# Performance work log

Hardware: AMD Instinct MI355X
Metric: run time of the kernel (lower is better)

Reference implementation:

```python
import jax, jax.numpy as jnp
import numpy as np

B, T, CH_IN = 4096, 8, 2048
C, N, K = 1024, 512, 5  # chennel, prototype length, n_prototypes/classes
EPS = 1e-8


def setup_inputs() -> dict:
    key = jax.random.key(0)
    ks = jax.random.split(key, 14)
    rn = lambda k, s: jax.random.normal(k, s, dtype=jnp.float32)
    return {
        "x": rn(ks[0], (B, T, CH_IN)),
        "static": rn(ks[1], (K, CH_IN, N)),
        "Wk": rn(ks[2], (C, CH_IN)) * 0.02, "bk": rn(ks[3], (C,)) * 0.02,
        "Wv": rn(ks[4], (C, CH_IN)) * 0.02, "bv": rn(ks[5], (C,)) * 0.02,
        "WEk": rn(ks[6], (C, CH_IN)) * 0.02, "bEk": rn(ks[7], (C,)) * 0.02,
        "WEv": rn(ks[8], (C, CH_IN)) * 0.02, "bEv": rn(ks[9], (C,)) * 0.02,
        "Ww": rn(ks[10], (1, C)) * 0.02, "bw": rn(ks[11], (1,)) * 0.02,
        "Wout": rn(ks[12], (K, 2 * C)) * 0.02, "bout": rn(ks[13], (K,)) * 0.02,
    }


def reference(x, static, Wk, bk, Wv, bv, WEk, bEk, WEv, bEv, Ww, bw, Wout, bout):
    # last frame only: [B, ch_in]
    x_last = x[:, -1, :]
    # 1x1 convs on a length-1 sequence == plain linear layers
    k = x_last @ Wk.T + bk  # [B, C]
    v = x_last @ Wv.T + bv  # [B, C]
    # project all 5 static prototypes at once: [K, C, N]
    Ek = jnp.einsum('ci,kin->kcn', WEk, static) + bEk[None, :, None]
    Ev = jnp.einsum('ci,kin->kcn', WEv, static) + bEv[None, :, None]
    # cosine similarity along channel dim (torch eps=1e-8)
    kn = k / jnp.maximum(jnp.linalg.norm(k, axis=1, keepdims=True), EPS)
    Ekn = Ek / jnp.maximum(jnp.linalg.norm(Ek, axis=1, keepdims=True), EPS)
    sim = jnp.einsum('bc,kcn->bkn', kn, Ekn)          # [B, K, N]
    w = jax.nn.softmax(sim, axis=-1)                  # softmax over prototypes' N entries
    # weighted sum of Ev per prototype -> feature_E [B, C, K]
    feature_E = jnp.einsum('kcn,bkn->bck', Ev, w)
    # scalar gate per prototype via conv2_1_W, then sigmoid
    fw = jax.nn.sigmoid(jnp.einsum('c,bck->bk', Ww[0], feature_E) + bw[0])  # [B, K]
    fE = jnp.einsum('bck,bk->bc', feature_E, fw)      # [B, C]
    out = jax.nn.relu(jnp.concatenate([v, fE], axis=1))  # [B, 2C]
    out = out @ Wout.T + bout                          # [B, K]
    return out[:, :, None]                             # [B, K, 1] matching torch conv1d output
```

## Files before the change

### kernel.cpp

```cpp
#include <hip/hip_runtime.h>
#include <hip/hip_bf16.h>

#define BB 4096
#define TT 8
#define CHIN 2048
#define CC 1024
#define NN 512
#define KK 5
#define KN (KK*NN)

typedef __bf16 bf16x8 __attribute__((ext_vector_type(8)));
typedef float  f32x4  __attribute__((ext_vector_type(4)));

#define TM 128
#define TN 128
#define BK 64

__device__ __forceinline__ void gload_lds16(const __hip_bfloat16* g, __hip_bfloat16* l) {
    __builtin_amdgcn_global_load_lds(
        (__attribute__((address_space(1))) void*)const_cast<__hip_bfloat16*>(g),
        (__attribute__((address_space(3))) void*)l,
        16, 0, 0);
}

__global__ __launch_bounds__(256) void gemm_abt(
    const __hip_bfloat16* __restrict__ A, int lda,
    const __hip_bfloat16* __restrict__ BT, int ldb,
    float* __restrict__ Cmat, int ldc,
    int M, int N, int Kdim,
    const float* __restrict__ bias_col)
{
    __shared__ __align__(16) __hip_bfloat16 As[TM * BK];
    __shared__ __align__(16) __hip_bfloat16 Bs[TN * BK];

    const int tid  = threadIdx.x;
    const int wave = tid >> 6;
    const int lane = tid & 63;
    const int wm = (wave >> 1) * 64;
    const int wn = (wave & 1) * 64;
    const int bm = blockIdx.y * TM;
    const int bn = blockIdx.x * TN;

    const int srow = tid >> 3;
    const int scol = (tid & 7) * 8;

    const __hip_bfloat16* Ag = A  + (size_t)bm * lda;
    const __hip_bfloat16* Bg = BT + (size_t)bn * ldb;

    f32x4 acc[4][4];
    #pragma unroll
    for (int i = 0; i < 4; ++i)
        #pragma unroll
        for (int j = 0; j < 4; ++j)
            acc[i][j] = {0.f, 0.f, 0.f, 0.f};

    for (int k0 = 0; k0 < Kdim; k0 += BK) {
        #pragma unroll
        for (int r = 0; r < 4; ++r) {
            int row = srow + r * 32;
            gload_lds16(Ag + (size_t)row * lda + k0 + scol, &As[row * BK + scol]);
        }
        #pragma unroll
        for (int r = 0; r < 4; ++r) {
            int row = srow + r * 32;
            gload_lds16(Bg + (size_t)row * ldb + k0 + scol, &Bs[row * BK + scol]);
        }
        __syncthreads();

        #pragma unroll
        for (int kk = 0; kk < BK; kk += 32) {
            const int koff = kk + (lane >> 4) * 8;
            const int arow = wm + (lane & 15);
            const int brow = wn + (lane & 15);
            bf16x8 aFrag[4], bFrag[4];
            #pragma unroll
            for (int i = 0; i < 4; ++i)
                aFrag[i] = *(const bf16x8*)(&As[(arow + i * 16) * BK + koff]);
            #pragma unroll
            for (int j = 0; j < 4; ++j)
                bFrag[j] = *(const bf16x8*)(&Bs[(brow + j * 16) * BK + koff]);
            #pragma unroll
            for (int i = 0; i < 4; ++i)
                #pragma unroll
                for (int j = 0; j < 4; ++j)
                    acc[i][j] = __builtin_amdgcn_mfma_f32_16x16x32_bf16(
                        aFrag[i], bFrag[j], acc[i][j], 0, 0, 0);
        }
        __syncthreads();
    }

    const int quad = lane >> 4;
    #pragma unroll
    for (int i = 0; i < 4; ++i) {
        #pragma unroll
        for (int j = 0; j < 4; ++j) {
            const int col = bn + wn + j * 16 + (lane & 15);
            const float bc = bias_col ? bias_col[col] : 0.f;
            #pragma unroll
            for (int r = 0; r < 4; ++r) {
                const int row = bm + wm + i * 16 + quad * 4 + r;
                Cmat[(size_t)row * ldc + col] = acc[i][j][r] + bc;
            }
        }
    }
}

__global__ __launch_bounds__(256) void cast_f32_bf16(const float* __restrict__ in,
                                                     __hip_bfloat16* __restrict__ out, int n)
{
    const int idx = (blockIdx.x * 256 + threadIdx.x) * 4;
    if (idx >= n) return;
    const float4 vv = *(const float4*)(in + idx);
    union { __hip_bfloat16 h[4]; unsigned long long u; } pk;
    pk.h[0] = (__hip_bfloat16)vv.x; pk.h[1] = (__hip_bfloat16)vv.y;
    pk.h[2] = (__hip_bfloat16)vv.z; pk.h[3] = (__hip_bfloat16)vv.w;
    *(unsigned long long*)(out + idx) = pk.u;
}

__global__ __launch_bounds__(256) void cast_xlast(const float* __restrict__ x,
                                                  __hip_bfloat16* __restrict__ xb)
{
    const int b = blockIdx.y;
    const int i = (blockIdx.x * 256 + threadIdx.x) * 4;
    const float4 vv = *(const float4*)(x + ((size_t)b * TT + TT - 1) * CHIN + i);
    union { __hip_bfloat16 h[4]; unsigned long long u; } pk;
    pk.h[0] = (__hip_bfloat16)vv.x; pk.h[1] = (__hip_bfloat16)vv.y;
    pk.h[2] = (__hip_bfloat16)vv.z; pk.h[3] = (__hip_bfloat16)vv.w;
    *(unsigned long long*)(xb + (size_t)b * CHIN + i) = pk.u;
}

__global__ __launch_bounds__(256) void concat_bias(const float* __restrict__ a,
                                                   const float* __restrict__ b,
                                                   float* __restrict__ out)
{
    const int i = blockIdx.x * 256 + threadIdx.x;
    out[i] = (i < CC) ? a[i] : b[i - CC];
}

__global__ void transpose_static(const float* __restrict__ st,
                                 __hip_bfloat16* __restrict__ stT)
{
    __shared__ float tile[32][33];
    const int k  = blockIdx.z;
    const int i0 = blockIdx.x * 32;
    const int n0 = blockIdx.y * 32;
    const int tx = threadIdx.x, ty = threadIdx.y;
    #pragma unroll
    for (int r = 0; r < 32; r += 8)
        tile[ty + r][tx] = st[((size_t)k * CHIN + i0 + ty + r) * NN + n0 + tx];
    __syncthreads();
    #pragma unroll
    for (int r = 0; r < 32; r += 8)
        stT[((size_t)k * NN + n0 + ty + r) * CHIN + i0 + tx] = (__hip_bfloat16)tile[tx][ty + r];
}

__global__ void transpose_bf16(const __hip_bfloat16* __restrict__ in,
                               __hip_bfloat16* __restrict__ outp)
{
    __shared__ __hip_bfloat16 tile[32][33];
    const int c0  = blockIdx.x * 32;
    const int kn0 = blockIdx.y * 32;
    const int tx = threadIdx.x, ty = threadIdx.y;
    #pragma unroll
    for (int r = 0; r < 32; r += 8)
        tile[ty + r][tx] = in[(size_t)(kn0 + ty + r) * CC + c0 + tx];
    __syncthreads();
    #pragma unroll
    for (int r = 0; r < 32; r += 8)
        outp[(size_t)(c0 + ty + r) * KN + kn0 + tx] = tile[tx][ty + r];
}

__global__ __launch_bounds__(256) void rownorm(const float* __restrict__ in, int in_ld,
                                               __hip_bfloat16* __restrict__ out, int cols)
{
    const int row = blockIdx.x;
    const float* p = in + (size_t)row * in_ld;
    float s = 0.f;
    for (int c = threadIdx.x; c < cols; c += 256) { float v = p[c]; s += v * v; }
    #pragma unroll
    for (int o = 32; o > 0; o >>= 1) s += __shfl_down(s, o, 64);
    __shared__ float red[4];
    if ((threadIdx.x & 63) == 0) red[threadIdx.x >> 6] = s;
    __syncthreads();
    const float tot = red[0] + red[1] + red[2] + red[3];
    const float inv = 1.f / fmaxf(sqrtf(tot), 1e-8f);
    for (int c = threadIdx.x; c < cols; c += 256)
        out[(size_t)row * cols + c] = (__hip_bfloat16)(p[c] * inv);
}

__global__ __launch_bounds__(256) void prep_gv(const float* __restrict__ Ekv,
                                               const float* __restrict__ Ww,
                                               float* __restrict__ g,
                                               __hip_bfloat16* __restrict__ EvT)
{
    const int kn = blockIdx.x;
    const float* p = Ekv + (size_t)kn * (2 * CC) + CC;
    float s = 0.f;
    for (int c = threadIdx.x; c < CC; c += 256) {
        const float v = p[c];
        s += Ww[c] * v;
        EvT[(size_t)kn * CC + c] = (__hip_bfloat16)v;
    }
    #pragma unroll
    for (int o = 32; o > 0; o >>= 1) s += __shfl_down(s, o, 64);
    __shared__ float red[4];
    if ((threadIdx.x & 63) == 0) red[threadIdx.x >> 6] = s;
    __syncthreads();
    if (threadIdx.x == 0) g[kn] = red[0] + red[1] + red[2] + red[3];
}

__global__ __launch_bounds__(64) void softmax_u(const float* __restrict__ sim,
                                                const float* __restrict__ g,
                                                const float* __restrict__ bw,
                                                __hip_bfloat16* __restrict__ u)
{
    const int bk = blockIdx.x;
    const int b = bk / KK, k = bk % KK;
    const float* sp = sim + (size_t)b * KN + k * NN;
    const float* gp = g + k * NN;
    const int lane = threadIdx.x;

    float vals[8];
    float m = -1e30f;
    #pragma unroll
    for (int j = 0; j < 8; ++j) { vals[j] = sp[lane + 64 * j]; m = fmaxf(m, vals[j]); }
    #pragma unroll
    for (int o = 32; o > 0; o >>= 1) m = fmaxf(m, __shfl_xor(m, o, 64));
    float sum = 0.f;
    #pragma unroll
    for (int j = 0; j < 8; ++j) { vals[j] = expf(vals[j] - m); sum += vals[j]; }
    #pragma unroll
    for (int o = 32; o > 0; o >>= 1) sum += __shfl_xor(sum, o, 64);
    const float inv = 1.f / sum;
    float dot = 0.f;
    #pragma unroll
    for (int j = 0; j < 8; ++j) { vals[j] *= inv; dot += vals[j] * gp[lane + 64 * j]; }
    #pragma unroll
    for (int o = 32; o > 0; o >>= 1) dot += __shfl_xor(dot, o, 64);
    const float fw = 1.f / (1.f + expf(-(dot + bw[0])));
    __hip_bfloat16* up = u + (size_t)b * KN + k * NN;
    #pragma unroll
    for (int j = 0; j < 8; ++j) up[lane + 64 * j] = (__hip_bfloat16)(vals[j] * fw);
}

__global__ __launch_bounds__(256) void final_out(const float* __restrict__ kv,
                                                 const float* __restrict__ fE,
                                                 const float* __restrict__ Wout,
                                                 const float* __restrict__ bout,
                                                 float* __restrict__ out)
{
    const int b = blockIdx.x;
    const float* vp = kv + (size_t)b * (2 * CC) + CC;
    float acc[KK] = {0.f, 0.f, 0.f, 0.f, 0.f};
    for (int c = threadIdx.x; c < CC; c += 256) {
        const float rv = fmaxf(vp[c], 0.f);
        const float rf = fmaxf(fE[(size_t)b * CC + c], 0.f);
        #pragma unroll
        for (int kk = 0; kk < KK; ++kk)
            acc[kk] += Wout[kk * 2 * CC + c] * rv
                     + Wout[kk * 2 * CC + CC + c] * rf;
    }
    __shared__ float red[KK][4];
    const int lane = threadIdx.x & 63, wave = threadIdx.x >> 6;
    #pragma unroll
    for (int kk = 0; kk < KK; ++kk) {
        float s = acc[kk];
        #pragma unroll
        for (int o = 32; o > 0; o >>= 1) s += __shfl_down(s, o, 64);
        if (lane == 0) red[kk][wave] = s;
    }
    __syncthreads();
    if (threadIdx.x < KK) {
        float s = red[threadIdx.x][0] + red[threadIdx.x][1]
                + red[threadIdx.x][2] + red[threadIdx.x][3];
        out[(size_t)b * KK + threadIdx.x] = s + bout[threadIdx.x];
    }
}

extern "C" void kernel_launch(void* const* d_in, const int* in_sizes, int n_in,
                              void* d_out, int out_size, void* d_ws, size_t ws_size,
                              hipStream_t stream)
{
    const float* x    = (const float*)d_in[0];
    const float* stat = (const float*)d_in[1];
    const float* Wk   = (const float*)d_in[2];
    const float* bk   = (const float*)d_in[3];
    const float* Wv   = (const float*)d_in[4];
    const float* bv   = (const float*)d_in[5];
    const float* WEk  = (const float*)d_in[6];
    const float* bEk  = (const float*)d_in[7];
    const float* WEv  = (const float*)d_in[8];
    const float* bEv  = (const float*)d_in[9];
    const float* Ww   = (const float*)d_in[10];
    const float* bw   = (const float*)d_in[11];
    const float* Wout = (const float*)d_in[12];
    const float* bout = (const float*)d_in[13];
    float* out = (float*)d_out;
    char* ws = (char*)d_ws;

    __hip_bfloat16* xb      = (__hip_bfloat16*)(ws + 0);
    __hip_bfloat16* Wkvb    = (__hip_bfloat16*)(ws + 16777216);
    __hip_bfloat16* WEkvb   = (__hip_bfloat16*)(ws + 25165824);
    __hip_bfloat16* staticT = (__hip_bfloat16*)(ws + 33554432);
    float*          Ekv     = (float*)(ws + 44040192);
    __hip_bfloat16* EknT    = (__hip_bfloat16*)(ws + 65011712);
    __hip_bfloat16* EvT     = (__hip_bfloat16*)(ws + 70254592);
    __hip_bfloat16* EvC     = (__hip_bfloat16*)(ws + 75497472);
    float*          g       = (float*)(ws + 80740352);
    float*          kv      = (float*)(ws + 80750592);
    __hip_bfloat16* kn      = (__hip_bfloat16*)(ws + 114305024);
    float*          sim     = (float*)(ws + 122693632);
    __hip_bfloat16* u       = (__hip_bfloat16*)(ws + 164636672);
    float*          fE      = (float*)(ws + 185608192);
    float*          bkv     = (float*)(ws + 202385408);
    float*          bEkv    = (float*)(ws + 202393600);

    const int WN = CC * CHIN;

    cast_f32_bf16<<<WN / 1024, 256, 0, stream>>>(Wk,  Wkvb,       WN);
    cast_f32_bf16<<<WN / 1024, 256, 0, stream>>>(Wv,  Wkvb + WN,  WN);
    cast_f32_bf16<<<WN / 1024, 256, 0, stream>>>(WEk, WEkvb,      WN);
    cast_f32_bf16<<<WN / 1024, 256, 0, stream>>>(WEv, WEkvb + WN, WN);
    cast_xlast<<<dim3(CHIN / 1024, BB), 256, 0, stream>>>(x, xb);
    concat_bias<<<2 * CC / 256, 256, 0, stream>>>(bk, bv, bkv);
    concat_bias<<<2 * CC / 256, 256, 0, stream>>>(bEk, bEv, bEkv);
    transpose_static<<<dim3(CHIN / 32, NN / 32, KK), dim3(32, 8), 0, stream>>>(stat, staticT);

    gemm_abt<<<dim3(2 * CC / TN, KN / TM), 256, 0, stream>>>(
        staticT, CHIN, WEkvb, CHIN, Ekv, 2 * CC, KN, 2 * CC, CHIN, bEkv);
    rownorm<<<KN, 256, 0, stream>>>(Ekv, 2 * CC, EknT, CC);
    prep_gv<<<KN, 256, 0, stream>>>(Ekv, Ww, g, EvT);
    transpose_bf16<<<dim3(CC / 32, KN / 32), dim3(32, 8), 0, stream>>>(EvT, EvC);
    gemm_abt<<<dim3(2 * CC / TN, BB / TM), 256, 0, stream>>>(
        xb, CHIN, Wkvb, CHIN, kv, 2 * CC, BB, 2 * CC, CHIN, bkv);
    rownorm<<<BB, 256, 0, stream>>>(kv, 2 * CC, kn, CC);
    gemm_abt<<<dim3(KN / TN, BB / TM), 256, 0, stream>>>(
        kn, CC, EknT, CC, sim, KN, BB, KN, CC, nullptr);
    softmax_u<<<BB * KK, 64, 0, stream>>>(sim, g, bw, u);
    gemm_abt<<<dim3(CC / TN, BB / TM), 256, 0, stream>>>(
        u, KN, EvC, KN, fE, CC, BB, CC, KN, nullptr);
    final_out<<<BB, 256, 0, stream>>>(kv, fE, Wout, bout, out);
}
```

Measured before the change: 629.9 us.

## Replace GEMM with 256x256 double-buffered swizzled 8-wave kernel, fuse and split-K

```diff
diff --git a/kernel.cpp b/kernel.cpp
--- a/kernel.cpp
+++ b/kernel.cpp
@@ -12,98 +12,235 @@
 typedef __bf16 bf16x8 __attribute__((ext_vector_type(8)));
 typedef float  f32x4  __attribute__((ext_vector_type(4)));
 
-#define TM 128
-#define TN 128
-#define BK 64
+#define BM 256
+#define BN 256
 
 __device__ __forceinline__ void gload_lds16(const __hip_bfloat16* g, __hip_bfloat16* l) {
     __builtin_amdgcn_global_load_lds(
         (__attribute__((address_space(1))) void*)const_cast<__hip_bfloat16*>(g),
-        (__attribute__((address_space(3))) void*)l,
-        16, 0, 0);
-}
-
-__global__ __launch_bounds__(256) void gemm_abt(
-    const __hip_bfloat16* __restrict__ A, int lda,
-    const __hip_bfloat16* __restrict__ BT, int ldb,
+        (__attribute__((address_space(3))) void*)l, 16, 0, 0);
+}
+
+__device__ __forceinline__ void stage_half(const __hip_bfloat16* __restrict__ g, int ldg,
+                                           __hip_bfloat16* l, int tid)
+{
+    #pragma unroll
+    for (int q = 0; q < 2; ++q) {
+        const int P   = q * 8192 + tid * 16;
+        const int row = P >> 7;
+        const int bc  = (P & 127) ^ ((row & 7) << 4);
+        gload_lds16(g + (size_t)row * ldg + (bc >> 1),
+                    (__hip_bfloat16*)((char*)l + P));
+    }
+}
+
+__device__ __forceinline__ bf16x8 lds_read_swz(const __hip_bfloat16* base, int row, int kbyte)
+{
+    int off = row * 128 + kbyte;
+    off ^= (row & 7) << 4;
+    return *(const bf16x8*)((const char*)base + off);
+}
+
+__device__ __forceinline__ void gemm8p_body(
+    const __hip_bfloat16* __restrict__ Ag, int lda,
+    const __hip_bfloat16* __restrict__ Bg, int ldb,
     float* __restrict__ Cmat, int ldc,
-    int M, int N, int Kdim,
-    const float* __restrict__ bias_col)
-{
-    __shared__ __align__(16) __hip_bfloat16 As[TM * BK];
-    __shared__ __align__(16) __hip_bfloat16 Bs[TN * BK];
+    int ntiles,
+    const float* __restrict__ bias_col,
+    int bm, int bn)
+{
+    __shared__ __align__(16) __hip_bfloat16 As[2][BM * 64];
+    __shared__ __align__(16) __hip_bfloat16 Bs[2][BN * 64];
 
     const int tid  = threadIdx.x;
     const int wave = tid >> 6;
     const int lane = tid & 63;
-    const int wm = (wave >> 1) * 64;
-    const int wn = (wave & 1) * 64;
-    const int bm = blockIdx.y * TM;
-    const int bn = blockIdx.x * TN;
-
-    const int srow = tid >> 3;
-    const int scol = (tid & 7) * 8;
-
-    const __hip_bfloat16* Ag = A  + (size_t)bm * lda;
-    const __hip_bfloat16* Bg = BT + (size_t)bn * ldb;
-
-    f32x4 acc[4][4];
-    #pragma unroll
-    for (int i = 0; i < 4; ++i)
+    const int wrow = (wave >> 2) * 128;
+    const int wcol = (wave & 3) * 64;
+    const int fr   = lane & 15;
+    const int kb0  = (lane >> 4) * 16;
+
+    const __hip_bfloat16* Arow = Ag + (size_t)bm * lda;
+    const __hip_bfloat16* Brow = Bg + (size_t)bn * ldb;
+
+    f32x4 acc[8][4];
+    #pragma unroll
+    for (int i = 0; i < 8; ++i)
         #pragma unroll
         for (int j = 0; j < 4; ++j)
             acc[i][j] = {0.f, 0.f, 0.f, 0.f};
 
-    for (int k0 = 0; k0 < Kdim; k0 += BK) {
-        #pragma unroll
-        for (int r = 0; r < 4; ++r) {
-            int row = srow + r * 32;
-            gload_lds16(Ag + (size_t)row * lda + k0 + scol, &As[row * BK + scol]);
+    bf16x8 a[4][2];
+    bf16x8 bfr[4][2];
+
+    stage_half(Arow,                       lda, &As[0][0],        tid);
+    stage_half(Arow + (size_t)128 * lda,   lda, &As[0][128 * 64], tid);
+    stage_half(Brow,                       ldb, &Bs[0][0],        tid);
+    stage_half(Brow + (size_t)128 * ldb,   ldb, &Bs[0][128 * 64], tid);
+    if (ntiles > 1) {
+        stage_half(Brow + 64,                     ldb, &Bs[1][0],        tid);
+        stage_half(Brow + (size_t)128 * ldb + 64, ldb, &Bs[1][128 * 64], tid);
+        asm volatile("s_waitcnt vmcnt(4)" ::: "memory");
+    } else {
+        asm volatile("s_waitcnt vmcnt(0)" ::: "memory");
+    }
+    __builtin_amdgcn_s_barrier();
+    __builtin_amdgcn_sched_barrier(0);
+
+    for (int T = 0; T < ntiles; ++T) {
+        const __hip_bfloat16* Abuf = &As[T & 1][0];
+        const __hip_bfloat16* Bbuf = &Bs[T & 1][0];
+
+        #pragma unroll
+        for (int i = 0; i < 4; ++i)
+            #pragma unroll
+            for (int k2 = 0; k2 < 2; ++k2)
+                a[i][k2] = lds_read_swz(Abuf, wrow + i * 16 + fr, k2 * 64 + kb0);
+        #pragma unroll
+        for (int j = 0; j < 2; ++j)
+            #pragma unroll
+            for (int k2 = 0; k2 < 2; ++k2)
+                bfr[j][k2] = lds_read_swz(Bbuf, wcol + j * 16 + fr, k2 * 64 + kb0);
+        if (T + 1 < ntiles)
+            stage_half(Arow + (size_t)(T + 1) * 64, lda, &As[(T + 1) & 1][0], tid);
+        __builtin_amdgcn_s_barrier();
+        asm volatile("s_waitcnt lgkmcnt(0)" ::: "memory");
+        __builtin_amdgcn_sched_barrier(0);
+        __builtin_amdgcn_s_setprio(1);
+        #pragma unroll
+        for (int i = 0; i < 4; ++i)
+            #pragma unroll
+            for (int j = 0; j < 2; ++j)
+                #pragma unroll
+                for (int k2 = 0; k2 < 2; ++k2)
+                    acc[i][j] = __builtin_amdgcn_mfma_f32_16x16x32_bf16(
+                        a[i][k2], bfr[j][k2], acc[i][j], 0, 0, 0);
+        __builtin_amdgcn_s_setprio(0);
+        __builtin_amdgcn_s_barrier();
+        __builtin_amdgcn_sched_barrier(0);
+
+        #pragma unroll
+        for (int j = 2; j < 4; ++j)
+            #pragma unroll
+            for (int k2 = 0; k2 < 2; ++k2)
+                bfr[j][k2] = lds_read_swz(Bbuf, wcol + j * 16 + fr, k2 * 64 + kb0);
+        if (T + 1 < ntiles)
+            stage_half(Arow + (size_t)128 * lda + (size_t)(T + 1) * 64, lda,
+                       &As[(T + 1) & 1][128 * 64], tid);
+        __builtin_amdgcn_s_barrier();
+        asm volatile("s_waitcnt lgkmcnt(0)" ::: "memory");
+        __builtin_amdgcn_sched_barrier(0);
+        __builtin_amdgcn_s_setprio(1);
+        #pragma unroll
+        for (int i = 0; i < 4; ++i)
+            #pragma unroll
+            for (int j = 2; j < 4; ++j)
+                #pragma unroll
+                for (int k2 = 0; k2 < 2; ++k2)
+                    acc[i][j] = __builtin_amdgcn_mfma_f32_16x16x32_bf16(
+                        a[i][k2], bfr[j][k2], acc[i][j], 0, 0, 0);
+        __builtin_amdgcn_s_setprio(0);
+        __builtin_amdgcn_s_barrier();
+        __builtin_amdgcn_sched_barrier(0);
+
+        #pragma unroll
+        for (int i = 0; i < 4; ++i)
+            #pragma unroll
+            for (int k2 = 0; k2 < 2; ++k2)
+                a[i][k2] = lds_read_swz(Abuf, wrow + 64 + i * 16 + fr, k2 * 64 + kb0);
+        if (T + 2 < ntiles)
+            stage_half(Brow + (size_t)(T + 2) * 64, ldb, &Bs[T & 1][0], tid);
+        __builtin_amdgcn_s_barrier();
+        asm volatile("s_waitcnt lgkmcnt(0)" ::: "memory");
+        __builtin_amdgcn_sched_barrier(0);
+        __builtin_amdgcn_s_setprio(1);
+        #pragma unroll
+        for (int i = 0; i < 4; ++i)
+            #pragma unroll
+            for (int j = 2; j < 4; ++j)
+                #pragma unroll
+                for (int k2 = 0; k2 < 2; ++k2)
+                    acc[i + 4][j] = __builtin_amdgcn_mfma_f32_16x16x32_bf16(
+                        a[i][k2], bfr[j][k2], acc[i + 4][j], 0, 0, 0);
+        __builtin_amdgcn_s_setprio(0);
+        __builtin_amdgcn_s_barrier();
+        __builtin_amdgcn_sched_barrier(0);
+
+        if (T + 2 < ntiles) {
+            stage_half(Brow + (size_t)128 * ldb + (size_t)(T + 2) * 64, ldb,
+                       &Bs[T & 1][128 * 64], tid);
+            asm volatile("s_waitcnt vmcnt(4)" ::: "memory");
+        } else if (T + 1 < ntiles) {
+            asm volatile("s_waitcnt vmcnt(0)" ::: "memory");
         }
-        #pragma unroll
-        for (int r = 0; r < 4; ++r) {
-            int row = srow + r * 32;
-            gload_lds16(Bg + (size_t)row * ldb + k0 + scol, &Bs[row * BK + scol]);
-        }
-        __syncthreads();
-
-        #pragma unroll
-        for (int kk = 0; kk < BK; kk += 32) {
-            const int koff = kk + (lane >> 4) * 8;
-            const int arow = wm + (lane & 15);
-            const int brow = wn + (lane & 15);
-            bf16x8 aFrag[4], bFrag[4];
-            #pragma unroll
-            for (int i = 0; i < 4; ++i)
-                aFrag[i] = *(const bf16x8*)(&As[(arow + i * 16) * BK + koff]);
-            #pragma unroll
-            for (int j = 0; j < 4; ++j)
-                bFrag[j] = *(const bf16x8*)(&Bs[(brow + j * 16) * BK + koff]);
-            #pragma unroll
-            for (int i = 0; i < 4; ++i)
+        __builtin_amdgcn_s_barrier();
+        __builtin_amdgcn_sched_barrier(0);
+        __builtin_amdgcn_s_setprio(1);
+        #pragma unroll
+        for (int i = 0; i < 4; ++i)
+            #pragma unroll
+            for (int j = 0; j < 2; ++j)
                 #pragma unroll
-                for (int j = 0; j < 4; ++j)
-                    acc[i][j] = __builtin_amdgcn_mfma_f32_16x16x32_bf16(
-                        aFrag[i], bFrag[j], acc[i][j], 0, 0, 0);
-        }
-        __syncthreads();
+                for (int k2 = 0; k2 < 2; ++k2)
+                    acc[i + 4][j] = __builtin_amdgcn_mfma_f32_16x16x32_bf16(
+                        a[i][k2], bfr[j][k2], acc[i + 4][j], 0, 0, 0);
+        __builtin_amdgcn_s_setprio(0);
+        __builtin_amdgcn_s_barrier();
+        __builtin_amdgcn_sched_barrier(0);
     }
 
     const int quad = lane >> 4;
     #pragma unroll
-    for (int i = 0; i < 4; ++i) {
+    for (int i = 0; i < 8; ++i) {
         #pragma unroll
         for (int j = 0; j < 4; ++j) {
-            const int col = bn + wn + j * 16 + (lane & 15);
+            const int col = bn + wcol + j * 16 + fr;
             const float bc = bias_col ? bias_col[col] : 0.f;
             #pragma unroll
             for (int r = 0; r < 4; ++r) {
-                const int row = bm + wm + i * 16 + quad * 4 + r;
+                const int row = bm + wrow + i * 16 + quad * 4 + r;
                 Cmat[(size_t)row * ldc + col] = acc[i][j][r] + bc;
             }
         }
     }
 }
+
+__global__ __launch_bounds__(512) void gemm8p_dual(
+    const __hip_bfloat16* __restrict__ A0, const __hip_bfloat16* __restrict__ B0,
+    float* __restrict__ C0, const float* __restrict__ bias0, int mt0,
+    const __hip_bfloat16* __restrict__ A1, const __hip_bfloat16* __restrict__ B1,
+    float* __restrict__ C1, const float* __restrict__ bias1)
+{
+    const int by = blockIdx.y;
+    const bool s = by >= mt0;
+    gemm8p_body(s ? A1 : A0, CHIN, s ? B1 : B0, CHIN,
+                s ? C1 : C0, 2 * CC, CHIN / 64,
+                s ? bias1 : bias0,
+                (s ? by - mt0 : by) * BM, blockIdx.x * BN);
+}
+
+__global__ __launch_bounds__(512) void gemm8p(
+    const __hip_bfloat16* __restrict__ A, int lda,
+    const __hip_bfloat16* __restrict__ BT, int ldb,
+    float* __restrict__ C, int ldc, int ntiles,
+    const float* __restrict__ bias)
+{
+    gemm8p_body(A, lda, BT, ldb, C, ldc, ntiles, bias,
+                blockIdx.y * BM, blockIdx.x * BN);
+}
+
+__global__ __launch_bounds__(512) void gemm8p_splitk(
+    const __hip_bfloat16* __restrict__ A, int lda,
+    const __hip_bfloat16* __restrict__ BT, int ldb,
+    float* __restrict__ C0, float* __restrict__ C1, int ldc, int khalf_tiles)
+{
+    const int z = blockIdx.z;
+    gemm8p_body(A + (size_t)z * khalf_tiles * 64, lda,
+                BT + (size_t)z * khalf_tiles * 64, ldb,
+                z ? C1 : C0, ldc, khalf_tiles, nullptr,
+                blockIdx.y * BM, blockIdx.x * BN);
+}
+
 
 __global__ __launch_bounds__(256) void cast_f32_bf16(const float* __restrict__ in,
                                                      __hip_bfloat16* __restrict__ out, int n)
@@ -244,7 +381,8 @@
 }
 
 __global__ __launch_bounds__(256) void final_out(const float* __restrict__ kv,
-                                                 const float* __restrict__ fE,
+                                                 const float* __restrict__ fE0,
+                                                 const float* __restrict__ fE1,
                                                  const float* __restrict__ Wout,
                                                  const float* __restrict__ bout,
                                                  float* __restrict__ out)
@@ -254,7 +392,7 @@
     float acc[KK] = {0.f, 0.f, 0.f, 0.f, 0.f};
     for (int c = threadIdx.x; c < CC; c += 256) {
         const float rv = fmaxf(vp[c], 0.f);
-        const float rf = fmaxf(fE[(size_t)b * CC + c], 0.f);
+        const float rf = fmaxf(fE0[(size_t)b * CC + c] + fE1[(size_t)b * CC + c], 0.f);
         #pragma unroll
         for (int kk = 0; kk < KK; ++kk)
             acc[kk] += Wout[kk * 2 * CC + c] * rv
@@ -314,6 +452,7 @@
     float*          fE      = (float*)(ws + 185608192);
     float*          bkv     = (float*)(ws + 202385408);
     float*          bEkv    = (float*)(ws + 202393600);
+    float*          fE2     = (float*)(ws + 202401792);
 
     const int WN = CC * CHIN;
 
@@ -326,18 +465,17 @@
     concat_bias<<<2 * CC / 256, 256, 0, stream>>>(bEk, bEv, bEkv);
     transpose_static<<<dim3(CHIN / 32, NN / 32, KK), dim3(32, 8), 0, stream>>>(stat, staticT);
 
-    gemm_abt<<<dim3(2 * CC / TN, KN / TM), 256, 0, stream>>>(
-        staticT, CHIN, WEkvb, CHIN, Ekv, 2 * CC, KN, 2 * CC, CHIN, bEkv);
+    gemm8p_dual<<<dim3(2 * CC / BN, KN / BM + BB / BM), 512, 0, stream>>>(
+        staticT, WEkvb, Ekv, bEkv, KN / BM,
+        xb, Wkvb, kv, bkv);
     rownorm<<<KN, 256, 0, stream>>>(Ekv, 2 * CC, EknT, CC);
     prep_gv<<<KN, 256, 0, stream>>>(Ekv, Ww, g, EvT);
     transpose_bf16<<<dim3(CC / 32, KN / 32), dim3(32, 8), 0, stream>>>(EvT, EvC);
-    gemm_abt<<<dim3(2 * CC / TN, BB / TM), 256, 0, stream>>>(
-        xb, CHIN, Wkvb, CHIN, kv, 2 * CC, BB, 2 * CC, CHIN, bkv);
     rownorm<<<BB, 256, 0, stream>>>(kv, 2 * CC, kn, CC);
-    gemm_abt<<<dim3(KN / TN, BB / TM), 256, 0, stream>>>(
-        kn, CC, EknT, CC, sim, KN, BB, KN, CC, nullptr);
+    gemm8p<<<dim3(KN / BN, BB / BM), 512, 0, stream>>>(
+        kn, CC, EknT, CC, sim, KN, CC / 64, nullptr);
     softmax_u<<<BB * KK, 64, 0, stream>>>(sim, g, bw, u);
-    gemm_abt<<<dim3(CC / TN, BB / TM), 256, 0, stream>>>(
-        u, KN, EvC, KN, fE, CC, BB, CC, KN, nullptr);
-    final_out<<<BB, 256, 0, stream>>>(kv, fE, Wout, bout, out);
-}
+    gemm8p_splitk<<<dim3(CC / BN, BB / BM, 2), 512, 0, stream>>>(
+        u, KN, EvC, KN, fE, fE2, CC, (KN / 2) / 64);
+    final_out<<<BB, 256, 0, stream>>>(kv, fE, fE2, Wout, bout, out);
+}
```

After: 567.8 us. 9.9% less time.
